# Performance work log

Hardware: AMD Instinct MI355X
Metric: run time of the kernel (lower is better)

## Reference

```python
import jax, jax.numpy as jnp
import numpy as np

S, B, D = 2048, 4, 1024

def setup_inputs() -> dict:
    key = jax.random.key(0)
    ks = jax.random.split(key, 7)
    std = 1.0 / np.sqrt(D)
    return {
        "x": jax.random.normal(ks[0], (S, B, D), dtype=jnp.float32),
        "Wq": jax.random.normal(ks[1], (D, D), dtype=jnp.float32) * std,
        "bq": jax.random.normal(ks[2], (D,), dtype=jnp.float32) * std,
        "Wk": jax.random.normal(ks[3], (D, D), dtype=jnp.float32) * std,
        "bk": jax.random.normal(ks[4], (D,), dtype=jnp.float32) * std,
        "Wv": jax.random.normal(ks[5], (D, D), dtype=jnp.float32) * std,
        "bv": jax.random.normal(ks[6], (D,), dtype=jnp.float32) * std,
    }

def reference(x, Wq, bq, Wk, bk, Wv, bv):
    # x: (S, B, D); flatten(start_dim=2) is a no-op for 3D input
    xf = jnp.transpose(x, (1, 0, 2))  # (B, S, D)
    # torch Linear: y = x @ W.T + b (W is (out, in))
    q = jnp.einsum('bsd,ed->bse', xf, Wq) + bq
    k = jnp.einsum('bsd,ed->bse', xf, Wk) + bk
    v = jnp.einsum('bsd,ed->bse', xf, Wv) + bv
    scale = 1.0 / jnp.sqrt(jnp.asarray(x.shape[-1], dtype=x.dtype))
    scores = jnp.einsum('bqd,bkd->bqk', q, k) * scale  # (B, S, S)
    attn = jax.nn.softmax(scores, axis=-1)
    weighted = jnp.einsum('bqk,bkd->bqd', attn, v)  # (B, S, D)
    # Faithful to torch.reshape(weighted, x.shape): reshape, NOT transpose back
    return jnp.reshape(weighted, x.shape)
```

## Files before the change

### kernel.cpp

```cpp
#include <hip/hip_runtime.h>
#include <math.h>

typedef float  f4     __attribute__((ext_vector_type(4)));
typedef float  f32x4  __attribute__((ext_vector_type(4)));
typedef short  bf16x8 __attribute__((ext_vector_type(8)));
typedef unsigned short u16x8 __attribute__((ext_vector_type(8)));

#define S_ 2048
#define B_ 4
#define D_ 1024

__device__ __forceinline__ unsigned short f2bf(float f) {
    unsigned u = __builtin_bit_cast(unsigned, f);
    u = (u + 0x7FFFu + ((u >> 16) & 1u)) >> 16;
    return (unsigned short)u;
}

#define GLOAD16(gsrc, ldst) \
    __builtin_amdgcn_global_load_lds((const __attribute__((address_space(1))) void*)(gsrc), \
                                     (__attribute__((address_space(3))) void*)(ldst), 16, 0, 0)


__global__ __launch_bounds__(128)
void convert_x(const float* __restrict__ x, unsigned short* __restrict__ xb)
{
    const int bid = blockIdx.x;
    const int b = bid & (B_ - 1);
    const int s = bid >> 2;
    const int t = threadIdx.x;
    const float* in = x + (size_t)bid * D_ + t * 8;
    unsigned short* out = xb + ((size_t)b * S_ + s) * D_ + t * 8;
    f4 lo = *(const f4*)in;
    f4 hi = *(const f4*)(in + 4);
    u16x8 o;
#pragma unroll
    for (int j = 0; j < 4; j++) { o[j] = f2bf(lo[j]); o[4 + j] = f2bf(hi[j]); }
    *(u16x8*)out = o;
}

__global__ __launch_bounds__(256)
void convert_w(const float* __restrict__ W0, const float* __restrict__ W1,
               const float* __restrict__ W2, unsigned short* __restrict__ dst)
{
    const float* src = (blockIdx.z == 0) ? W0 : (blockIdx.z == 1) ? W1 : W2;
    unsigned short* d = dst + (size_t)blockIdx.z * D_ * D_;
    size_t i = ((size_t)blockIdx.x * 256 + threadIdx.x) * 8;
    f4 lo = *(const f4*)(src + i);
    f4 hi = *(const f4*)(src + i + 4);
    u16x8 o;
#pragma unroll
    for (int j = 0; j < 4; j++) { o[j] = f2bf(lo[j]); o[4 + j] = f2bf(hi[j]); }
    *(u16x8*)(d + i) = o;
}

__global__ __launch_bounds__(256)
void convert_bias(const float* __restrict__ b0, const float* __restrict__ b1,
                  const float* __restrict__ b2, float* __restrict__ bcat)
{
    int i = blockIdx.x * 256 + threadIdx.x;
    int z = i >> 10, j = i & 1023;
    bcat[i] = (z == 0) ? b0[j] : (z == 1) ? b1[j] : b2[j];
}

__global__ __launch_bounds__(256)
void transpose_v(const unsigned short* __restrict__ qkv, unsigned short* __restrict__ vt)
{
    __shared__ unsigned short tile[64][72];
    const int t = threadIdx.x;
    const int s0 = blockIdx.x * 64, d0 = blockIdx.y * 64, b = blockIdx.z;
    const int rr = t >> 3, c8 = (t & 7) * 8;
#pragma unroll
    for (int p = 0; p < 2; p++) {
        int r = rr + p * 32;
        u16x8 v = *(const u16x8*)(qkv + ((size_t)b * S_ + s0 + r) * 3072 + 2048 + d0 + c8);
#pragma unroll
        for (int j = 0; j < 8; j++) tile[r][c8 + j] = v[j];
    }
    __syncthreads();
#pragma unroll
    for (int p = 0; p < 2; p++) {
        int r = rr + p * 32;
        u16x8 o;
#pragma unroll
        for (int j = 0; j < 8; j++) o[j] = tile[c8 + j][r];
        *(u16x8*)(vt + ((size_t)b * D_ + d0 + r) * S_ + s0 + c8) = o;
    }
}

template<int BM, int BN, int WM, int WN, bool BIAS, bool OBF16>
__global__ __launch_bounds__(WM*WN*64, 2)
void gemm2(const unsigned short* __restrict__ A, const unsigned short* __restrict__ B,
           const float* __restrict__ bias, void* __restrict__ C,
           int lda, int ldb, int ldc, int K, float alpha,
           size_t sA, size_t sB, size_t sC)
{
    constexpr int T   = WM * WN * 64;
    constexpr int WTM = BM / WM, WTN = BN / WN;
    constexpr int MR  = WTM / 16, NR = WTN / 16;
    constexpr int MH  = MR / 2,  NH = NR / 2;
    constexpr int ABYTES = BM * 128;
    constexpr int BUFB   = (BM + BN) * 128;

    __shared__ char sm[2 * BUFB] __attribute__((aligned(128)));

    const int t  = threadIdx.x;
    const int w  = t >> 6, ln = t & 63;
    const int wr = w / WN, wc = w % WN;
    const int c15 = ln & 15, k16 = ln >> 4;

    const int gx  = gridDim.x;
    const int nwg = gx * gridDim.y;
    const int l0  = blockIdx.y * gx + blockIdx.x;
    const int cpx = nwg >> 3;
    const int lsw = (l0 & 7) * cpx + (l0 >> 3);
    const int m0  = (lsw % gx) * BM;
    const int n0  = (lsw / gx) * BN;

    const unsigned short* Ab = A + blockIdx.z * sA;
    const unsigned short* Bb = B + blockIdx.z * sB;

    const char* srcp[8];
    int ldso[8];
#pragma unroll
    for (int l = 0; l < 8; l++) {
        int p = (l * T + t) * 16;
        int q = p ^ (((p >> 9) & 3) << 5);
        if (q < ABYTES) {
            int r = q >> 7, cb = q & 127;
            srcp[l] = (const char*)(Ab + (size_t)(m0 + r) * lda) + cb;
        } else {
            int q2 = q - ABYTES;
            int r = q2 >> 7, cb = q2 & 127;
            srcp[l] = (const char*)(Bb + (size_t)(n0 + r) * ldb) + cb;
        }
        ldso[l] = (l * T + (t & ~63)) * 16;
    }

    const int rbA   = (wr * WTM + c15) * 128 + k16 * 16;
    const int xorA  = ((rbA >> 9) & 3) << 5;
    const int bA0   = rbA ^ xorA;
    const int bA1   = (rbA + 64) ^ xorA;
    const int rbB   = (wc * WTN + c15) * 128 + k16 * 16;
    const int xorB  = ((rbB >> 9) & 3) << 5;
    const int bB0   = ABYTES + (rbB ^ xorB);
    const int bB1   = ABYTES + ((rbB + 64) ^ xorB);

    f32x4 acc[MR][NR];
#pragma unroll
    for (int i = 0; i < MR; i++)
#pragma unroll
        for (int j = 0; j < NR; j++) acc[i][j] = (f32x4)0.f;

#pragma unroll
    for (int l = 0; l < 8; l++) GLOAD16(srcp[l], sm + ldso[l]);

    const int NT = K >> 6;
    int cur = 0;
    for (int kt = 0; kt < NT; ++kt) {
        asm volatile("s_waitcnt vmcnt(0)" ::: "memory");
        __builtin_amdgcn_s_barrier();
        const char* rb  = sm + cur * BUFB;
        char*       wbuf = sm + (cur ^ 1) * BUFB;
        const size_t kbn = (size_t)(kt + 1) * 128;
        const bool  st  = (kt + 1 < NT);

        bf16x8 Bfr[2][NH][2];
        int ph = 0;
#pragma unroll
        for (int mh = 0; mh < 2; mh++) {
            bf16x8 Afr[MH][2];
#pragma unroll
            for (int i = 0; i < MH; i++) {
                Afr[i][0] = *(const bf16x8*)(rb + bA0 + (mh * MH + i) * 2048);
                Afr[i][1] = *(const bf16x8*)(rb + bA1 + (mh * MH + i) * 2048);
            }
#pragma unroll
            for (int nh = 0; nh < 2; nh++) {
                if (st && ph == 0) {
                    GLOAD16(srcp[0] + kbn, wbuf + ldso[0]);
                    GLOAD16(srcp[1] + kbn, wbuf + ldso[1]);
                    GLOAD16(srcp[2] + kbn, wbuf + ldso[2]);
                    GLOAD16(srcp[3] + kbn, wbuf + ldso[3]);
                }
                if (st && ph == 1) {
                    GLOAD16(srcp[4] + kbn, wbuf + ldso[4]);
                    GLOAD16(srcp[5] + kbn, wbuf + ldso[5]);
                    GLOAD16(srcp[6] + kbn, wbuf + ldso[6]);
                    GLOAD16(srcp[7] + kbn, wbuf + ldso[7]);
                }
                if (mh == 0) {
#pragma unroll
                    for (int j = 0; j < NH; j++) {
                        Bfr[nh][j][0] = *(const bf16x8*)(rb + bB0 + (nh * NH + j) * 2048);
                        Bfr[nh][j][1] = *(const bf16x8*)(rb + bB1 + (nh * NH + j) * 2048);
                    }
                }
                __builtin_amdgcn_s_setprio(1);
#pragma unroll
                for (int i = 0; i < MH; i++)
#pragma unroll
                    for (int j = 0; j < NH; j++) {
                        acc[mh*MH+i][nh*NH+j] = __builtin_amdgcn_mfma_f32_16x16x32_bf16(
                            Afr[i][0], Bfr[nh][j][0], acc[mh*MH+i][nh*NH+j], 0, 0, 0);
                        acc[mh*MH+i][nh*NH+j] = __builtin_amdgcn_mfma_f32_16x16x32_bf16(
                            Afr[i][1], Bfr[nh][j][1], acc[mh*MH+i][nh*NH+j], 0, 0, 0);
                    }
                __builtin_amdgcn_s_setprio(0);
                ph++;
            }
        }
        cur ^= 1;
    }

    float bvv[NR];
#pragma unroll
    for (int j = 0; j < NR; j++)
        bvv[j] = BIAS ? bias[n0 + wc * WTN + j * 16 + c15] : 0.f;

#pragma unroll
    for (int mi = 0; mi < MR; mi++) {
        const int row = m0 + wr * WTM + mi * 16 + k16 * 4;
#pragma unroll
        for (int nj = 0; nj < NR; nj++) {
            const int col = n0 + wc * WTN + nj * 16 + c15;
#pragma unroll
            for (int r = 0; r < 4; r++) {
                float vv = acc[mi][nj][r] * alpha + bvv[nj];
                if (OBF16)
                    ((unsigned short*)C + blockIdx.z * sC)[(size_t)(row + r) * ldc + col] = f2bf(vv);
                else
                    ((float*)C + blockIdx.z * sC)[(size_t)(row + r) * ldc + col] = vv;
            }
        }
    }
}

__global__ __launch_bounds__(256)
void softmax_rows(float* __restrict__ P)
{
    float* p = P + (size_t)blockIdx.x * S_;
    const int t = threadIdx.x;

    f4 v0 = *(f4*)&p[t * 8];
    f4 v1 = *(f4*)&p[t * 8 + 4];

    float mx = v0[0];
#pragma unroll
    for (int j = 0; j < 4; j++) { mx = fmaxf(mx, v0[j]); mx = fmaxf(mx, v1[j]); }
#pragma unroll
    for (int off = 32; off > 0; off >>= 1) mx = fmaxf(mx, __shfl_xor(mx, off));

    __shared__ float rmax[4], rsum[4];
    if ((t & 63) == 0) rmax[t >> 6] = mx;
    __syncthreads();
    mx = fmaxf(fmaxf(rmax[0], rmax[1]), fmaxf(rmax[2], rmax[3]));

    float sum = 0.f;
#pragma unroll
    for (int j = 0; j < 4; j++) {
        v0[j] = __expf(v0[j] - mx); sum += v0[j];
        v1[j] = __expf(v1[j] - mx); sum += v1[j];
    }
#pragma unroll
    for (int off = 32; off > 0; off >>= 1) sum += __shfl_xor(sum, off);
    if ((t & 63) == 0) rsum[t >> 6] = sum;
    __syncthreads();
    sum = rsum[0] + rsum[1] + rsum[2] + rsum[3];

    float inv = 1.f / sum;
    unsigned short* ob = (unsigned short*)p;
    u16x8 o;
#pragma unroll
    for (int j = 0; j < 4; j++) { o[j] = f2bf(v0[j] * inv); o[4 + j] = f2bf(v1[j] * inv); }
    __syncthreads();
    *(u16x8*)&ob[t * 8] = o;
}


extern "C" void kernel_launch(void* const* d_in, const int* in_sizes, int n_in,
                              void* d_out, int out_size, void* d_ws, size_t ws_size,
                              hipStream_t stream)
{
    const float* x  = (const float*)d_in[0];
    const float* Wq = (const float*)d_in[1];
    const float* bq = (const float*)d_in[2];
    const float* Wk = (const float*)d_in[3];
    const float* bk = (const float*)d_in[4];
    const float* Wv = (const float*)d_in[5];
    const float* bv = (const float*)d_in[6];
    float* out = (float*)d_out;

    const size_t nTok = (size_t)B_ * S_;
    char* ws = (char*)d_ws;

    unsigned short* xb   = (unsigned short*)ws;   ws += nTok * D_ * 2;
    unsigned short* wcat = (unsigned short*)ws;   ws += (size_t)3 * D_ * D_ * 2;
    float*          bcat = (float*)ws;            ws += 3 * D_ * 4;
    unsigned short* qkv  = (unsigned short*)ws;   ws += nTok * 3 * D_ * 2;
    unsigned short* vt   = (unsigned short*)ws;   ws += nTok * D_ * 2;
    float*          sc   = (float*)ws;            ws += (size_t)B_ * S_ * S_ * 4;
    if ((size_t)(ws - (char*)d_ws) > ws_size) return;

    convert_x<<<dim3(S_ * B_), dim3(128), 0, stream>>>(x, xb);
    convert_w<<<dim3(512, 1, 3), dim3(256), 0, stream>>>(Wq, Wk, Wv, wcat);
    convert_bias<<<dim3(12), dim3(256), 0, stream>>>(bq, bk, bv, bcat);

    gemm2<256, 256, 2, 4, true, true><<<dim3(32, 12, 1), dim3(512), 0, stream>>>(
        xb, wcat, bcat, qkv, D_, D_, 3 * D_, D_, 1.f, 0, 0, 0);

    transpose_v<<<dim3(S_ / 64, D_ / 64, B_), dim3(256), 0, stream>>>(qkv, vt);

    gemm2<256, 256, 2, 4, false, false><<<dim3(8, 8, B_), dim3(512), 0, stream>>>(
        qkv, qkv + D_, nullptr, sc, 3 * D_, 3 * D_, S_, D_, 0.03125f,
        (size_t)S_ * 3 * D_, (size_t)S_ * 3 * D_, (size_t)S_ * S_);

    softmax_rows<<<dim3(B_ * S_), dim3(256), 0, stream>>>(sc);

    gemm2<128, 128, 2, 2, false, false><<<dim3(16, 8, B_), dim3(256), 0, stream>>>(
        (const unsigned short*)sc, vt, nullptr, out, 2 * S_, S_, D_, S_, 1.f,
        (size_t)S_ * S_ * 2, (size_t)D_ * S_, (size_t)S_ * D_);
}
```

Before: 267.4 us.

## Unify GEMMs into one 512-thread kernel with reordered LDS staging and batch-mapped PV tiles

Replaces the templated gemm2 with gemm8, which always uses 8 waves. It issues all next-tile global-to-LDS loads up front, interleaved with fragment reads and four MFMA quads. The QKV projection moves to 256x128 tiles, giving a larger grid. The PV GEMM moves to 256x128 tiles with the batch folded into the M dimension (PVMAP), so a flattened 2D grid replaces the per-batch z dimension. The aim is better latency hiding and occupancy, at the cost of different tile shapes and possible register pressure.

```diff
diff --git a/kernel.cpp b/kernel.cpp
--- a/kernel.cpp
+++ b/kernel.cpp
@@ -19,6 +19,8 @@
 #define GLOAD16(gsrc, ldst) \
     __builtin_amdgcn_global_load_lds((const __attribute__((address_space(1))) void*)(gsrc), \
                                      (__attribute__((address_space(3))) void*)(ldst), 16, 0, 0)
+
+#define VMCNT(n) asm volatile("s_waitcnt vmcnt(%0)" :: "n"(n) : "memory")
 
 
 __global__ __launch_bounds__(128)
@@ -87,25 +89,29 @@
     }
 }
 
-template<int BM, int BN, int WM, int WN, bool BIAS, bool OBF16>
-__global__ __launch_bounds__(WM*WN*64, 2)
-void gemm2(const unsigned short* __restrict__ A, const unsigned short* __restrict__ B,
+template<int BM, int BN, bool BIAS, bool OBF16, bool PVMAP>
+__global__ __launch_bounds__(512, 2)
+void gemm8(const char* __restrict__ A_, int ldab,
+           const char* __restrict__ B_in, int ldbb,
            const float* __restrict__ bias, void* __restrict__ C,
-           int lda, int ldb, int ldc, int K, float alpha,
-           size_t sA, size_t sB, size_t sC)
-{
-    constexpr int T   = WM * WN * 64;
-    constexpr int WTM = BM / WM, WTN = BN / WN;
+           int ldc, int K, float alpha,
+           size_t zAb, size_t zBb, size_t zCe)
+{
+    constexpr int T   = 512;
+    constexpr int WTM = BM / 2, WTN = BN / 4;
     constexpr int MR  = WTM / 16, NR = WTN / 16;
-    constexpr int MH  = MR / 2,  NH = NR / 2;
-    constexpr int ABYTES = BM * 128;
-    constexpr int BUFB   = (BM + BN) * 128;
+    constexpr int MH  = MR / 2, NRH = NR / 2;
+    constexpr int ABYTES = BM * 128, BBYTES = BN * 128;
+    constexpr int BUFB = ABYTES + BBYTES;
+    constexpr int L   = BUFB / (T * 16);
+    constexpr int LA2 = ABYTES / 2 / (T * 16);
+    constexpr int LB2 = BBYTES / 2 / (T * 16);
 
     __shared__ char sm[2 * BUFB] __attribute__((aligned(128)));
 
     const int t  = threadIdx.x;
     const int w  = t >> 6, ln = t & 63;
-    const int wr = w / WN, wc = w % WN;
+    const int wr = w >> 2, wc = w & 3;
     const int c15 = ln & 15, k16 = ln >> 4;
 
     const int gx  = gridDim.x;
@@ -116,107 +122,98 @@
     const int m0  = (lsw % gx) * BM;
     const int n0  = (lsw / gx) * BN;
 
-    const unsigned short* Ab = A + blockIdx.z * sA;
-    const unsigned short* Bb = B + blockIdx.z * sB;
-
-    const char* srcp[8];
-    int ldso[8];
-#pragma unroll
-    for (int l = 0; l < 8; l++) {
-        int p = (l * T + t) * 16;
-        int q = p ^ (((p >> 9) & 3) << 5);
-        if (q < ABYTES) {
-            int r = q >> 7, cb = q & 127;
-            srcp[l] = (const char*)(Ab + (size_t)(m0 + r) * lda) + cb;
-        } else {
-            int q2 = q - ABYTES;
-            int r = q2 >> 7, cb = q2 & 127;
-            srcp[l] = (const char*)(Bb + (size_t)(n0 + r) * ldb) + cb;
-        }
-        ldso[l] = (l * T + (t & ~63)) * 16;
-    }
-
-    const int rbA   = (wr * WTM + c15) * 128 + k16 * 16;
-    const int xorA  = ((rbA >> 9) & 3) << 5;
-    const int bA0   = rbA ^ xorA;
-    const int bA1   = (rbA + 64) ^ xorA;
-    const int rbB   = (wc * WTN + c15) * 128 + k16 * 16;
-    const int xorB  = ((rbB >> 9) & 3) << 5;
-    const int bB0   = ABYTES + (rbB ^ xorB);
-    const int bB1   = ABYTES + ((rbB + 64) ^ xorB);
-
+    const int bz = PVMAP ? (m0 >> 11) : blockIdx.z;
+    const char* Ab = A_  + (size_t)bz * zAb;
+    const char* Bb = B_in + (size_t)bz * zBb;
+    const int   am0 = PVMAP ? (m0 & (S_ - 1)) : m0;
+
+    const int p0 = t * 16;
+    const int q0 = p0 ^ (((p0 >> 9) & 3) << 5);
+    const int r0 = q0 >> 7, cb0 = q0 & 127;
+    const char* srcA = Ab + (size_t)(am0 + r0) * ldab + cb0;
+    const char* srcB = Bb + (size_t)(n0  + r0) * ldbb + cb0;
+    const int wub = (t & ~63) * 16;
+
+#define STAGE(KB, WB) \
+    _Pragma("unroll") \
+    for (int j = 0; j < L; ++j) { \
+        if (j < LA2) { \
+            GLOAD16(srcA + (size_t)(j * 64) * ldab + (KB), (WB) + j * 8192 + wub); \
+        } else if (j < LA2 + LB2) { \
+            int l = j - LA2; \
+            GLOAD16(srcB + (size_t)(l * 64) * ldbb + (KB), (WB) + ABYTES + l * 8192 + wub); \
+        } else if (j < LA2 + 2 * LB2) { \
+            int l = j - LA2 - LB2; \
+            GLOAD16(srcB + (size_t)(BN / 2 + l * 64) * ldbb + (KB), (WB) + ABYTES + BBYTES / 2 + l * 8192 + wub); \
+        } else { \
+            int l = j - LA2 - 2 * LB2; \
+            GLOAD16(srcA + (size_t)(BM / 2 + l * 64) * ldab + (KB), (WB) + ABYTES / 2 + l * 8192 + wub); \
+        } \
+    }
+
+    const int qA  = (wr * WTM + c15) * 128 + k16 * 16;
+    const int xA  = ((qA >> 9) & 3) << 5;
+    const int bA0 = qA ^ xA;
+    const int bA1 = (qA + 64) ^ xA;
+    const int qB  = ABYTES + (wc * WTN + c15) * 128 + k16 * 16;
+    const int xB  = ((qB >> 9) & 3) << 5;
+    const int bB0 = qB ^ xB;
+    const int bB1 = (qB + 64) ^ xB;
+
+    bf16x8 Af[MH][2], Bf[2][NRH][2];
     f32x4 acc[MR][NR];
 #pragma unroll
     for (int i = 0; i < MR; i++)
 #pragma unroll
         for (int j = 0; j < NR; j++) acc[i][j] = (f32x4)0.f;
 
-#pragma unroll
-    for (int l = 0; l < 8; l++) GLOAD16(srcp[l], sm + ldso[l]);
+#define RDA(mh, RB) \
+    _Pragma("unroll") for (int f = 0; f < MH; ++f) { \
+        Af[f][0] = *(const bf16x8*)((RB) + bA0 + (mh) * (MH * 2048) + f * 2048); \
+        Af[f][1] = *(const bf16x8*)((RB) + bA1 + (mh) * (MH * 2048) + f * 2048); }
+#define RDB(nh, RB) \
+    _Pragma("unroll") for (int g = 0; g < NRH; ++g) { \
+        Bf[nh][g][0] = *(const bf16x8*)((RB) + bB0 + (nh) * (NRH * 2048) + g * 2048); \
+        Bf[nh][g][1] = *(const bf16x8*)((RB) + bB1 + (nh) * (NRH * 2048) + g * 2048); }
+#define QUAD(mh, nh) \
+    __builtin_amdgcn_s_setprio(1); \
+    _Pragma("unroll") for (int f = 0; f < MH; ++f) \
+    _Pragma("unroll") for (int g = 0; g < NRH; ++g) { \
+        acc[(mh)*MH+f][(nh)*NRH+g] = __builtin_amdgcn_mfma_f32_16x16x32_bf16( \
+            Af[f][0], Bf[nh][g][0], acc[(mh)*MH+f][(nh)*NRH+g], 0, 0, 0); \
+        acc[(mh)*MH+f][(nh)*NRH+g] = __builtin_amdgcn_mfma_f32_16x16x32_bf16( \
+            Af[f][1], Bf[nh][g][1], acc[(mh)*MH+f][(nh)*NRH+g], 0, 0, 0); } \
+    __builtin_amdgcn_s_setprio(0);
+
+    STAGE(0, sm);
 
     const int NT = K >> 6;
     int cur = 0;
     for (int kt = 0; kt < NT; ++kt) {
-        asm volatile("s_waitcnt vmcnt(0)" ::: "memory");
+        VMCNT(0);
         __builtin_amdgcn_s_barrier();
-        const char* rb  = sm + cur * BUFB;
-        char*       wbuf = sm + (cur ^ 1) * BUFB;
+        const char* rb  = sm + (cur ? BUFB : 0);
+        char*       wb2 = sm + (cur ? 0 : BUFB);
         const size_t kbn = (size_t)(kt + 1) * 128;
-        const bool  st  = (kt + 1 < NT);
-
-        bf16x8 Bfr[2][NH][2];
-        int ph = 0;
-#pragma unroll
-        for (int mh = 0; mh < 2; mh++) {
-            bf16x8 Afr[MH][2];
-#pragma unroll
-            for (int i = 0; i < MH; i++) {
-                Afr[i][0] = *(const bf16x8*)(rb + bA0 + (mh * MH + i) * 2048);
-                Afr[i][1] = *(const bf16x8*)(rb + bA1 + (mh * MH + i) * 2048);
-            }
-#pragma unroll
-            for (int nh = 0; nh < 2; nh++) {
-                if (st && ph == 0) {
-                    GLOAD16(srcp[0] + kbn, wbuf + ldso[0]);
-                    GLOAD16(srcp[1] + kbn, wbuf + ldso[1]);
-                    GLOAD16(srcp[2] + kbn, wbuf + ldso[2]);
-                    GLOAD16(srcp[3] + kbn, wbuf + ldso[3]);
-                }
-                if (st && ph == 1) {
-                    GLOAD16(srcp[4] + kbn, wbuf + ldso[4]);
-                    GLOAD16(srcp[5] + kbn, wbuf + ldso[5]);
-                    GLOAD16(srcp[6] + kbn, wbuf + ldso[6]);
-                    GLOAD16(srcp[7] + kbn, wbuf + ldso[7]);
-                }
-                if (mh == 0) {
-#pragma unroll
-                    for (int j = 0; j < NH; j++) {
-                        Bfr[nh][j][0] = *(const bf16x8*)(rb + bB0 + (nh * NH + j) * 2048);
-                        Bfr[nh][j][1] = *(const bf16x8*)(rb + bB1 + (nh * NH + j) * 2048);
-                    }
-                }
-                __builtin_amdgcn_s_setprio(1);
-#pragma unroll
-                for (int i = 0; i < MH; i++)
-#pragma unroll
-                    for (int j = 0; j < NH; j++) {
-                        acc[mh*MH+i][nh*NH+j] = __builtin_amdgcn_mfma_f32_16x16x32_bf16(
-                            Afr[i][0], Bfr[nh][j][0], acc[mh*MH+i][nh*NH+j], 0, 0, 0);
-                        acc[mh*MH+i][nh*NH+j] = __builtin_amdgcn_mfma_f32_16x16x32_bf16(
-                            Afr[i][1], Bfr[nh][j][1], acc[mh*MH+i][nh*NH+j], 0, 0, 0);
-                    }
-                __builtin_amdgcn_s_setprio(0);
-                ph++;
-            }
-        }
+
+        RDA(0, rb); RDB(0, rb);
+        if (kt + 1 < NT) { STAGE(kbn, wb2); }
+        QUAD(0, 0);
+        RDB(1, rb);
+        QUAD(0, 1);
+        RDA(1, rb);
+        QUAD(1, 0);
+        QUAD(1, 1);
         cur ^= 1;
     }
+    VMCNT(0);
 
     float bvv[NR];
 #pragma unroll
     for (int j = 0; j < NR; j++)
         bvv[j] = BIAS ? bias[n0 + wc * WTN + j * 16 + c15] : 0.f;
 
+    char* Cb = (char*)C;
 #pragma unroll
     for (int mi = 0; mi < MR; mi++) {
         const int row = m0 + wr * WTM + mi * 16 + k16 * 4;
@@ -227,12 +224,16 @@
             for (int r = 0; r < 4; r++) {
                 float vv = acc[mi][nj][r] * alpha + bvv[nj];
                 if (OBF16)
-                    ((unsigned short*)C + blockIdx.z * sC)[(size_t)(row + r) * ldc + col] = f2bf(vv);
+                    ((unsigned short*)Cb + (PVMAP ? 0 : blockIdx.z * zCe))[(size_t)(row + r) * ldc + col] = f2bf(vv);
                 else
-                    ((float*)C + blockIdx.z * sC)[(size_t)(row + r) * ldc + col] = vv;
+                    ((float*)Cb + (PVMAP ? 0 : blockIdx.z * zCe))[(size_t)(row + r) * ldc + col] = vv;
             }
         }
     }
+#undef STAGE
+#undef RDA
+#undef RDB
+#undef QUAD
 }
 
 __global__ __launch_bounds__(256)
@@ -305,18 +306,19 @@
     convert_w<<<dim3(512, 1, 3), dim3(256), 0, stream>>>(Wq, Wk, Wv, wcat);
     convert_bias<<<dim3(12), dim3(256), 0, stream>>>(bq, bk, bv, bcat);
 
-    gemm2<256, 256, 2, 4, true, true><<<dim3(32, 12, 1), dim3(512), 0, stream>>>(
-        xb, wcat, bcat, qkv, D_, D_, 3 * D_, D_, 1.f, 0, 0, 0);
+    gemm8<256, 128, true, true, false><<<dim3(32, 24, 1), dim3(512), 0, stream>>>(
+        (const char*)xb, D_ * 2, (const char*)wcat, D_ * 2, bcat, qkv,
+        3 * D_, D_, 1.f, 0, 0, 0);
 
     transpose_v<<<dim3(S_ / 64, D_ / 64, B_), dim3(256), 0, stream>>>(qkv, vt);
 
-    gemm2<256, 256, 2, 4, false, false><<<dim3(8, 8, B_), dim3(512), 0, stream>>>(
-        qkv, qkv + D_, nullptr, sc, 3 * D_, 3 * D_, S_, D_, 0.03125f,
-        (size_t)S_ * 3 * D_, (size_t)S_ * 3 * D_, (size_t)S_ * S_);
+    gemm8<256, 256, false, false, false><<<dim3(8, 8, B_), dim3(512), 0, stream>>>(
+        (const char*)qkv, 3 * D_ * 2, (const char*)(qkv + D_), 3 * D_ * 2, nullptr, sc,
+        S_, D_, 0.03125f, (size_t)S_ * 3 * D_ * 2, (size_t)S_ * 3 * D_ * 2, (size_t)S_ * S_);
 
     softmax_rows<<<dim3(B_ * S_), dim3(256), 0, stream>>>(sc);
 
-    gemm2<128, 128, 2, 2, false, false><<<dim3(16, 8, B_), dim3(256), 0, stream>>>(
-        (const unsigned short*)sc, vt, nullptr, out, 2 * S_, S_, D_, S_, 1.f,
-        (size_t)S_ * S_ * 2, (size_t)D_ * S_, (size_t)S_ * D_);
-}
+    gemm8<256, 128, false, false, true><<<dim3(32, 8, 1), dim3(512), 0, stream>>>(
+        (const char*)sc, S_ * 4, (const char*)vt, S_ * 2, nullptr, out,
+        D_, S_, 1.f, (size_t)S_ * S_ * 4, (size_t)D_ * S_ * 2, 0);
+}
```

New measurement: 281.7 us. 5.4% more time.
